# Kernel tuning notes

Measured on AMD Instinct MI355X. Metric: run time of the kernel, lower is better.

The kernel has to match this reference:

```python
import jax, jax.numpy as jnp
import numpy as np

NUM_SEQ, B, T, F, S, OUT = 4, 256, 64, 32, 512, 1


def setup_inputs() -> dict:
    key = jax.random.key(0)
    k = jax.random.split(key, 6)
    return {
        "inputs": jax.random.normal(k[0], (NUM_SEQ, B, T, F), dtype=jnp.float32),
        "W_cell": jax.random.normal(k[1], (NUM_SEQ, F + S, S), dtype=jnp.float32) * 0.05,
        "b_cell": jnp.zeros((NUM_SEQ, S), dtype=jnp.float32),
        "W_comb": jax.random.normal(k[2], (NUM_SEQ - 1, 2 * S, 1), dtype=jnp.float32) * 0.05,
        "b_comb": jnp.zeros((NUM_SEQ - 1, 1), dtype=jnp.float32),
        "W_out": jax.random.normal(k[3], (S, OUT), dtype=jnp.float32) * 0.05,
    }


def reference(inputs, W_cell, b_cell, W_comb, b_comb, W_out):
    # inputs: [num_seq, B, T, F]. Lanes are processed sequentially; lane i>0
    # gates its running state against lane i-1's stored per-step states.
    num_seq, bsz = inputs.shape[0], inputs.shape[1]
    state_size = W_cell.shape[-1]
    prev_states = None  # [T, B, S] states of previous lane
    final_states = []
    for i in range(num_seq):
        xs = jnp.swapaxes(inputs[i], 0, 1)  # [T, B, F]
        Wc, bc = W_cell[i], b_cell[i]
        h0 = jnp.zeros((bsz, state_size), dtype=inputs.dtype)
        if i == 0:
            def step(h, xt, Wc=Wc, bc=bc):
                h_new = jnp.tanh(jnp.concatenate([xt, h], axis=-1) @ Wc + bc)
                return h_new, h_new
            _, states = jax.lax.scan(step, h0, xs)
        else:
            Wg, bg = W_comb[i - 1], b_comb[i - 1]
            def step(h, x, Wc=Wc, bc=bc, Wg=Wg, bg=bg):
                xt, ph = x
                w = jax.nn.sigmoid(jnp.concatenate([h, ph], axis=-1) @ Wg + bg)  # [B,1]
                hc = w * h + (1.0 - w) * ph
                h_new = jnp.tanh(jnp.concatenate([xt, hc], axis=-1) @ Wc + bc)
                return h_new, h_new
            _, states = jax.lax.scan(step, h0, (xs, prev_states))
        prev_states = states  # [T, B, S]
        final_states.append(states[-1])
    final = jnp.concatenate(final_states, axis=0)  # [num_seq*B, S]
    out = final @ W_out  # no bias, matching tf.layers.dense(use_bias=False)
    return out.reshape(-1, num_seq, W_out.shape[1])  # [B, num_seq, OUT]
```

## Files before the change

kernel.cpp:

```cpp
#include <hip/hip_runtime.h>
#include <math.h>

#define NSEQ 4
#define BATCH 256
#define T 64
#define FIN 32
#define S 512
#define KTOT 544

#define NT 512
#define NWG 256
#define RPG 16
#define SW 128
#define NSL 4
#define DEPTH 4
#define NKT 17

#define RING_SZ  (4ull * DEPTH * BATCH * S)
#define OUTP_OFF RING_SZ
#define CTL_OFF  (RING_SZ + 16384ull)

#define FLAG_MAGIC 0x13572468u

#define AS 552

typedef __attribute__((ext_vector_type(8))) short short8;
typedef __attribute__((ext_vector_type(4))) float f32x4;

__device__ __forceinline__ unsigned short bf_hi(float f) {
  return (unsigned short)(__float_as_uint(f) >> 16);
}
__device__ __forceinline__ float bf_hi_f(float f) {
  return __uint_as_float(__float_as_uint(f) & 0xFFFF0000u);
}

__device__ __forceinline__ unsigned ld_cnt(const unsigned* p) {
  return __hip_atomic_load(p, __ATOMIC_RELAXED, __HIP_MEMORY_SCOPE_AGENT);
}

__device__ __forceinline__ void cstore1(float* p, float v) {
  asm volatile("global_store_dword %0, %1, off sc0 sc1" :: "v"(p), "v"(v) : "memory");
}
__device__ __forceinline__ float cload1(const float* p) {
  float v;
  asm volatile("global_load_dword %0, %1, off sc0 sc1\n\ts_waitcnt vmcnt(0)"
               : "=v"(v) : "v"(p) : "memory");
  return v;
}
__device__ __forceinline__ void cload_row(float4* d, const float* p) {
  asm volatile(
      "global_load_dwordx4 %0, %4, off sc0 sc1\n\t"
      "global_load_dwordx4 %1, %4, off offset:512 sc0 sc1\n\t"
      "global_load_dwordx4 %2, %4, off offset:1024 sc0 sc1\n\t"
      "global_load_dwordx4 %3, %4, off offset:1536 sc0 sc1\n\t"
      "s_waitcnt vmcnt(0)"
      : "=&v"(d[0]), "=&v"(d[1]), "=&v"(d[2]), "=&v"(d[3])
      : "v"(p) : "memory");
}
__device__ __forceinline__ void cload_row2(float4* h, float4* q,
                                           const float* ph, const float* pp) {
  asm volatile(
      "global_load_dwordx4 %0, %8, off sc0 sc1\n\t"
      "global_load_dwordx4 %1, %8, off offset:512 sc0 sc1\n\t"
      "global_load_dwordx4 %2, %8, off offset:1024 sc0 sc1\n\t"
      "global_load_dwordx4 %3, %8, off offset:1536 sc0 sc1\n\t"
      "global_load_dwordx4 %4, %9, off sc0 sc1\n\t"
      "global_load_dwordx4 %5, %9, off offset:512 sc0 sc1\n\t"
      "global_load_dwordx4 %6, %9, off offset:1024 sc0 sc1\n\t"
      "global_load_dwordx4 %7, %9, off offset:1536 sc0 sc1\n\t"
      "s_waitcnt vmcnt(0)"
      : "=&v"(h[0]), "=&v"(h[1]), "=&v"(h[2]), "=&v"(h[3]),
        "=&v"(q[0]), "=&v"(q[1]), "=&v"(q[2]), "=&v"(q[3])
      : "v"(ph), "v"(pp) : "memory");
}

extern "C" __global__ void __launch_bounds__(NT, 1)
rnn_mfma(const float* __restrict__ x,
         const float* __restrict__ Wcell,
         const float* __restrict__ bcell,
         const float* __restrict__ Wcomb,
         const float* __restrict__ bcomb,
         const float* __restrict__ Wout,
         float* __restrict__ out,
         float* __restrict__ ws)
{
  const int b    = blockIdx.x;
  const int sl   = b & 3;
  const int gid  = b >> 2;
  const int lane = gid >> 4;
  const int grp  = gid & 15;
  const int r0 = grp * RPG, sb = sl * SW;
  const int tid = threadIdx.x;

  __shared__ __align__(16) unsigned short A1[RPG * AS];
  __shared__ __align__(16) unsigned short A2[RPG * AS];
  __shared__ float wg_lds[2 * S];
  __shared__ float obuf[128];
  __shared__ float fbuf[64];

  float* ring = ws;
  unsigned* ctl      = (unsigned*)(ws + CTL_OFF);
  unsigned* cnt_own  = ctl + gid * 32;
  unsigned* flg_own  = cnt_own + 16;
  unsigned* cnt_prod = ctl + (gid - 16) * 32;
  unsigned* cnt_cons = ctl + (gid + 16) * 32;

  if (sl == 0 && tid == 0) {
    __hip_atomic_store(cnt_own, 0u, __ATOMIC_RELAXED, __HIP_MEMORY_SCOPE_AGENT);
    __hip_atomic_store(flg_own, FLAG_MAGIC, __ATOMIC_RELEASE, __HIP_MEMORY_SCOPE_AGENT);
  }
  if (tid == 0) {
    while (__hip_atomic_load(flg_own, __ATOMIC_ACQUIRE, __HIP_MEMORY_SCOPE_AGENT) != FLAG_MAGIC)
      __builtin_amdgcn_s_sleep(1);
    if (lane > 0)
      while (__hip_atomic_load(cnt_prod + 16, __ATOMIC_ACQUIRE, __HIP_MEMORY_SCOPE_AGENT) != FLAG_MAGIC)
        __builtin_amdgcn_s_sleep(1);
    if (lane < 3)
      while (__hip_atomic_load(cnt_cons + 16, __ATOMIC_ACQUIRE, __HIP_MEMORY_SCOPE_AGENT) != FLAG_MAGIC)
        __builtin_amdgcn_s_sleep(1);
  }

  const float* Wc = Wcell + (size_t)lane * KTOT * S;
  const int wl = tid & 63, wt = tid >> 6;
  const int bn = wl & 15, q = wl >> 4;
  const int ncol = sb + wt * 16 + bn;
  short8 B1[NKT], B2[NKT];
  #pragma unroll
  for (int kt = 0; kt < NKT; ++kt) {
    short8 b1, b2;
    #pragma unroll
    for (int j = 0; j < 8; ++j) {
      const float w = Wc[(size_t)(kt * 32 + q * 8 + j) * S + ncol];
      b1[j] = (short)bf_hi(w);
      b2[j] = (short)bf_hi(w - bf_hi_f(w));
    }
    B1[kt] = b1; B2[kt] = b2;
  }
  const float bcv = bcell[lane * S + ncol];
  const float wov = Wout[ncol];
  for (int idx = tid; idx < 2 * S; idx += NT)
    wg_lds[idx] = (lane > 0) ? Wcomb[(size_t)(lane - 1) * 2 * S + idx] : 0.0f;
  const float bg = (lane > 0) ? bcomb[lane - 1] : 0.0f;
  const int grow = tid >> 5, gch = tid & 31;
  __syncthreads();

  float oacc[4] = {0.f, 0.f, 0.f, 0.f};

  for (int t = 0; t < T; ++t) {
    {
      const float f0 = x[(((size_t)lane * BATCH + r0 + grow) * T + t) * FIN + gch];
      A1[grow * AS + gch] = bf_hi(f0);
      A2[grow * AS + gch] = bf_hi(f0 - bf_hi_f(f0));
    }
    if (tid == 0) {
      if (t > 0)                  while (ld_cnt(cnt_own)  < 4u * (unsigned)t) {}
      if (lane > 0)               while (ld_cnt(cnt_prod) < 4u * (unsigned)(t + 1)) {}
      if (lane < 3 && t >= DEPTH) while (ld_cnt(cnt_cons) < 4u * (unsigned)(t - 3)) {}
    }
    __syncthreads();

    {
      const int row = grow;
      float4 hv[4], pv[4];
      const float* hb = ring + ((size_t)(lane * DEPTH + ((t - 1) & 3)) * BATCH + r0 + row) * S + gch * 4;
      const float* pb = ring + ((size_t)((lane - 1) * DEPTH + (t & 3)) * BATCH + r0 + row) * S + gch * 4;
      if (t > 0) {
        if (lane > 0) cload_row2(hv, pv, hb, pb);
        else          cload_row(hv, hb);
      } else {
        #pragma unroll
        for (int j = 0; j < 4; ++j) hv[j] = make_float4(0.f, 0.f, 0.f, 0.f);
        if (lane > 0) cload_row(pv, pb);
      }
      if (lane > 0) {
        float gs = 0.0f;
        #pragma unroll
        for (int j = 0; j < 4; ++j) {
          const float* wh = &wg_lds[j * 128 + gch * 4];
          const float* wp = wh + S;
          gs += hv[j].x * wh[0] + hv[j].y * wh[1] + hv[j].z * wh[2] + hv[j].w * wh[3];
          gs += pv[j].x * wp[0] + pv[j].y * wp[1] + pv[j].z * wp[2] + pv[j].w * wp[3];
        }
        gs += __shfl_xor(gs, 1);  gs += __shfl_xor(gs, 2);  gs += __shfl_xor(gs, 4);
        gs += __shfl_xor(gs, 8);  gs += __shfl_xor(gs, 16);
        const float w = 1.0f / (1.0f + __expf(-(gs + bg)));
        #pragma unroll
        for (int j = 0; j < 4; ++j) {
          hv[j].x = fmaf(w, hv[j].x - pv[j].x, pv[j].x);
          hv[j].y = fmaf(w, hv[j].y - pv[j].y, pv[j].y);
          hv[j].z = fmaf(w, hv[j].z - pv[j].z, pv[j].z);
          hv[j].w = fmaf(w, hv[j].w - pv[j].w, pv[j].w);
        }
      }
      #pragma unroll
      for (int j = 0; j < 4; ++j) {
        ushort4 h4, l4;
        h4.x = bf_hi(hv[j].x); l4.x = bf_hi(hv[j].x - bf_hi_f(hv[j].x));
        h4.y = bf_hi(hv[j].y); l4.y = bf_hi(hv[j].y - bf_hi_f(hv[j].y));
        h4.z = bf_hi(hv[j].z); l4.z = bf_hi(hv[j].z - bf_hi_f(hv[j].z));
        h4.w = bf_hi(hv[j].w); l4.w = bf_hi(hv[j].w - bf_hi_f(hv[j].w));
        const int ai = row * AS + 32 + j * 128 + gch * 4;
        *(ushort4*)&A1[ai] = h4;
        *(ushort4*)&A2[ai] = l4;
      }
    }
    __syncthreads();

    f32x4 acc = {0.f, 0.f, 0.f, 0.f};
    {
      const unsigned short* ar1 = &A1[bn * AS + q * 8];
      const unsigned short* ar2 = &A2[bn * AS + q * 8];
      #pragma unroll
      for (int kt = 0; kt < NKT; ++kt) {
        const short8 a1 = *(const short8*)(ar1 + kt * 32);
        const short8 a2 = *(const short8*)(ar2 + kt * 32);
        acc = __builtin_amdgcn_mfma_f32_16x16x32_bf16(a1, B1[kt], acc, 0, 0, 0);
        acc = __builtin_amdgcn_mfma_f32_16x16x32_bf16(a1, B2[kt], acc, 0, 0, 0);
        acc = __builtin_amdgcn_mfma_f32_16x16x32_bf16(a2, B1[kt], acc, 0, 0, 0);
      }
    }

    float* slot = ring + ((size_t)(lane * DEPTH + (t & 3)) * BATCH + r0) * S + sb;
    #pragma unroll
    for (int reg = 0; reg < 4; ++reg) {
      const float s2 = acc[reg] + bcv;
      const float aa = fabsf(s2), ee = __expf(2.0f * aa);
      const float tv = copysignf(1.0f - 2.0f / (ee + 1.0f), s2);
      cstore1(slot + (size_t)(q * 4 + reg) * S + wt * 16 + bn, tv);
      if (t == T - 1) oacc[reg] = tv * wov;
    }
    asm volatile("s_waitcnt vmcnt(0)" ::: "memory");
    __syncthreads();
    if (tid == 0)
      __hip_atomic_fetch_add(cnt_own, 1u, __ATOMIC_RELAXED, __HIP_MEMORY_SCOPE_AGENT);
  }

  #pragma unroll
  for (int reg = 0; reg < 4; ++reg) {
    float v = oacc[reg];
    v += __shfl_xor(v, 1); v += __shfl_xor(v, 2);
    v += __shfl_xor(v, 4); v += __shfl_xor(v, 8);
    if (bn == 0) obuf[wt * 16 + q * 4 + reg] = v;
  }
  __syncthreads();
  if (tid < 16) {
    float v = 0.0f;
    #pragma unroll
    for (int w = 0; w < 8; ++w) v += obuf[w * 16 + tid];
    cstore1(ws + OUTP_OFF + (size_t)((gid * 4 + sl) * 16 + tid), v);
  }
  asm volatile("s_waitcnt vmcnt(0)" ::: "memory");
  __syncthreads();
  if (tid == 0)
    __hip_atomic_fetch_add(cnt_own, 1u, __ATOMIC_RELAXED, __HIP_MEMORY_SCOPE_AGENT);
  if (sl == 0) {
    if (tid == 0)
      while (ld_cnt(cnt_own) < 4u * (unsigned)(T + 1)) {}
    __syncthreads();
    if (tid < 64) {
      const int sli = tid >> 4, r = tid & 15;
      fbuf[tid] = cload1(ws + OUTP_OFF + (size_t)((gid * 4 + sli) * 16 + r));
    }
    __syncthreads();
    if (tid < 16) {
      float s2 = 0.f;
      #pragma unroll
      for (int sli = 0; sli < 4; ++sli) s2 += fbuf[sli * 16 + tid];
      out[lane * BATCH + r0 + tid] = s2;
    }
  }
}

extern "C" void kernel_launch(void* const* d_in, const int* in_sizes, int n_in,
                              void* d_out, int out_size, void* d_ws, size_t ws_size,
                              hipStream_t stream) {
  (void)in_sizes; (void)n_in; (void)out_size; (void)ws_size;
  rnn_mfma<<<dim3(NWG), dim3(NT), 0, stream>>>(
      (const float*)d_in[0],
      (const float*)d_in[1],
      (const float*)d_in[2],
      (const float*)d_in[3],
      (const float*)d_in[4],
      (const float*)d_in[5],
      (float*)d_out,
      (float*)d_ws);
}
```

Before: 390.5 us.

## Replace atomic step counters with per-slice flag stores and remap blocks

Each workgroup now publishes its step progress by plain cache-bypassing stores into its own slot of a four-entry status vector, instead of doing an atomic add on a shared counter. Every thread polls its own, producer and consumer status vectors with three vector loads and takes the minimum, which removes the tid-0 spin and the barrier that followed it. Block indices are also remapped so that the lanes and slices of a row group are placed differently across the device. This trades atomic contention and the barrier for extra polling traffic from all threads, and relies on plain stores for ordering.

New measurement: 367.9 us. 5.8% less time.

```diff
diff --git a/kernel.cpp b/kernel.cpp
--- a/kernel.cpp
+++ b/kernel.cpp
@@ -12,7 +12,6 @@
 #define NWG 256
 #define RPG 16
 #define SW 128
-#define NSL 4
 #define DEPTH 4
 #define NKT 17
 
@@ -26,6 +25,7 @@
 
 typedef __attribute__((ext_vector_type(8))) short short8;
 typedef __attribute__((ext_vector_type(4))) float f32x4;
+typedef __attribute__((ext_vector_type(4))) unsigned u32x4;
 
 __device__ __forceinline__ unsigned short bf_hi(float f) {
   return (unsigned short)(__float_as_uint(f) >> 16);
@@ -33,11 +33,41 @@
 __device__ __forceinline__ float bf_hi_f(float f) {
   return __uint_as_float(__float_as_uint(f) & 0xFFFF0000u);
 }
-
-__device__ __forceinline__ unsigned ld_cnt(const unsigned* p) {
-  return __hip_atomic_load(p, __ATOMIC_RELAXED, __HIP_MEMORY_SCOPE_AGENT);
-}
-
+__device__ __forceinline__ unsigned umin4(u32x4 v) {
+  unsigned a = v[0] < v[1] ? v[0] : v[1];
+  unsigned b = v[2] < v[3] ? v[2] : v[3];
+  return a < b ? a : b;
+}
+
+__device__ __forceinline__ void cstoreu_glb(unsigned* p, unsigned v) {
+  asm volatile("global_store_dword %0, %1, off sc0 sc1" :: "v"(p), "v"(v) : "memory");
+}
+__device__ __forceinline__ void cstore4_glb(unsigned* p, u32x4 v) {
+  asm volatile("global_store_dwordx4 %0, %1, off sc0 sc1" :: "v"(p), "v"(v) : "memory");
+}
+__device__ __forceinline__ unsigned cldu_glb(const unsigned* p) {
+  unsigned v;
+  asm volatile("global_load_dword %0, %1, off sc0 sc1\n\ts_waitcnt vmcnt(0)"
+               : "=v"(v) : "v"(p) : "memory");
+  return v;
+}
+__device__ __forceinline__ u32x4 cld4_glb(const unsigned* p) {
+  u32x4 v;
+  asm volatile("global_load_dwordx4 %0, %1, off sc0 sc1\n\ts_waitcnt vmcnt(0)"
+               : "=v"(v) : "v"(p) : "memory");
+  return v;
+}
+__device__ __forceinline__ void cld3x4_glb(u32x4* a, u32x4* b, u32x4* c,
+                                           const unsigned* pa, const unsigned* pb,
+                                           const unsigned* pc) {
+  asm volatile(
+      "global_load_dwordx4 %0, %3, off sc0 sc1\n\t"
+      "global_load_dwordx4 %1, %4, off sc0 sc1\n\t"
+      "global_load_dwordx4 %2, %5, off sc0 sc1\n\t"
+      "s_waitcnt vmcnt(0)"
+      : "=&v"(*a), "=&v"(*b), "=&v"(*c)
+      : "v"(pa), "v"(pb), "v"(pc) : "memory");
+}
 __device__ __forceinline__ void cstore1(float* p, float v) {
   asm volatile("global_store_dword %0, %1, off sc0 sc1" :: "v"(p), "v"(v) : "memory");
 }
@@ -74,6 +104,7 @@
       : "v"(ph), "v"(pp) : "memory");
 }
 
+
 extern "C" __global__ void __launch_bounds__(NT, 1)
 rnn_mfma(const float* __restrict__ x,
          const float* __restrict__ Wcell,
@@ -85,10 +116,12 @@
          float* __restrict__ ws)
 {
   const int b    = blockIdx.x;
-  const int sl   = b & 3;
-  const int gid  = b >> 2;
-  const int lane = gid >> 4;
-  const int grp  = gid & 15;
+  const int o    = b >> 3;
+  const int grp  = (b & 7) + 8 * (o >> 4);
+  const int sub  = o & 15;
+  const int lane = sub >> 2;
+  const int sl   = sub & 3;
+  const int gid  = lane * 16 + grp;
   const int r0 = grp * RPG, sb = sl * SW;
   const int tid = threadIdx.x;
 
@@ -99,25 +132,26 @@
   __shared__ float fbuf[64];
 
   float* ring = ws;
-  unsigned* ctl      = (unsigned*)(ws + CTL_OFF);
-  unsigned* cnt_own  = ctl + gid * 32;
-  unsigned* flg_own  = cnt_own + 16;
-  unsigned* cnt_prod = ctl + (gid - 16) * 32;
-  unsigned* cnt_cons = ctl + (gid + 16) * 32;
+  unsigned* ctl     = (unsigned*)(ws + CTL_OFF);
+  unsigned* st_own  = ctl + gid * 64;
+  unsigned* st_prod = ctl + (gid - 16) * 64;
+  unsigned* st_cons = ctl + (gid + 16) * 64;
+  unsigned* st_mine = st_own + sl;
+  const unsigned* pp_poll = (lane > 0) ? st_prod : st_own;
+  const unsigned* pc_poll = (lane < 3) ? st_cons : st_own;
 
   if (sl == 0 && tid == 0) {
-    __hip_atomic_store(cnt_own, 0u, __ATOMIC_RELAXED, __HIP_MEMORY_SCOPE_AGENT);
-    __hip_atomic_store(flg_own, FLAG_MAGIC, __ATOMIC_RELEASE, __HIP_MEMORY_SCOPE_AGENT);
+    const u32x4 z = {0u, 0u, 0u, 0u};
+    cstore4_glb(st_own, z);
+    asm volatile("s_waitcnt vmcnt(0)" ::: "memory");
+    cstoreu_glb(st_own + 32, FLAG_MAGIC);
   }
   if (tid == 0) {
-    while (__hip_atomic_load(flg_own, __ATOMIC_ACQUIRE, __HIP_MEMORY_SCOPE_AGENT) != FLAG_MAGIC)
-      __builtin_amdgcn_s_sleep(1);
-    if (lane > 0)
-      while (__hip_atomic_load(cnt_prod + 16, __ATOMIC_ACQUIRE, __HIP_MEMORY_SCOPE_AGENT) != FLAG_MAGIC)
-        __builtin_amdgcn_s_sleep(1);
-    if (lane < 3)
-      while (__hip_atomic_load(cnt_cons + 16, __ATOMIC_ACQUIRE, __HIP_MEMORY_SCOPE_AGENT) != FLAG_MAGIC)
-        __builtin_amdgcn_s_sleep(1);
+    #pragma unroll
+    for (int l = 0; l < 4; ++l) {
+      const unsigned* f = ctl + (l * 16 + grp) * 64 + 32;
+      while (cldu_glb(f) != FLAG_MAGIC) __builtin_amdgcn_s_sleep(1);
+    }
   }
 
   const float* Wc = Wcell + (size_t)lane * KTOT * S;
@@ -152,12 +186,16 @@
       A1[grow * AS + gch] = bf_hi(f0);
       A2[grow * AS + gch] = bf_hi(f0 - bf_hi_f(f0));
     }
-    if (tid == 0) {
-      if (t > 0)                  while (ld_cnt(cnt_own)  < 4u * (unsigned)t) {}
-      if (lane > 0)               while (ld_cnt(cnt_prod) < 4u * (unsigned)(t + 1)) {}
-      if (lane < 3 && t >= DEPTH) while (ld_cnt(cnt_cons) < 4u * (unsigned)(t - 3)) {}
-    }
-    __syncthreads();
+    for (;;) {
+      u32x4 so, sp, sc;
+      cld3x4_glb(&so, &sp, &sc, st_own, pp_poll, pc_poll);
+      bool ok = true;
+      if (t > 0)                  ok &= (umin4(so) >= (unsigned)t);
+      if (lane > 0)               ok &= (umin4(sp) >= (unsigned)(t + 1));
+      if (lane < 3 && t >= DEPTH) ok &= (umin4(sc) >= (unsigned)(t - 3));
+      if (ok) break;
+      __builtin_amdgcn_s_sleep(1);
+    }
 
     {
       const int row = grow;
@@ -231,8 +269,7 @@
     }
     asm volatile("s_waitcnt vmcnt(0)" ::: "memory");
     __syncthreads();
-    if (tid == 0)
-      __hip_atomic_fetch_add(cnt_own, 1u, __ATOMIC_RELAXED, __HIP_MEMORY_SCOPE_AGENT);
+    if (tid == 0) cstoreu_glb(st_mine, (unsigned)(t + 1));
   }
 
   #pragma unroll
@@ -251,11 +288,10 @@
   }
   asm volatile("s_waitcnt vmcnt(0)" ::: "memory");
   __syncthreads();
-  if (tid == 0)
-    __hip_atomic_fetch_add(cnt_own, 1u, __ATOMIC_RELAXED, __HIP_MEMORY_SCOPE_AGENT);
+  if (tid == 0) cstoreu_glb(st_mine, (unsigned)(T + 1));
   if (sl == 0) {
     if (tid == 0)
-      while (ld_cnt(cnt_own) < 4u * (unsigned)(T + 1)) {}
+      while (umin4(cld4_glb(st_own)) < (unsigned)(T + 1)) __builtin_amdgcn_s_sleep(1);
     __syncthreads();
     if (tid < 64) {
       const int sli = tid >> 4, r = tid & 15;
```
